# Optimization experiments

Measured on AMD Instinct MI355X. Metric: run time of the kernel, lower is better.

Reference implementation:

```python
import jax, jax.numpy as jnp
import numpy as np

B, C, H, G, NCLS = 32, 256, 128, 128, 2  # graphs, nodes-per-graph==in_channels, hidden, matrix pool, classes
N = B * C                                # total nodes = 8192
E = 131072


def setup_inputs() -> dict:
    key = jax.random.key(0)
    ks = jax.random.split(key, 12)
    gain = 5.0 / 3.0
    xav = gain * np.sqrt(6.0 / (C + C))  # xavier_uniform bound for [C,C]
    return {
        "x": jax.random.normal(ks[0], (N, C), jnp.float32),
        "edge_index": jax.random.randint(ks[1], (2, E), 0, N),
        "graph_id": jax.random.randint(ks[2], (B,), 0, G),
        "batch": jnp.arange(N) // C,
        "pert_W": jax.random.uniform(ks[3], (G, C, C), jnp.float32, -xav, xav),
        "pert_b": jax.random.uniform(ks[4], (G, C, C), jnp.float32, -xav, xav),
        "mask_W": jax.random.uniform(ks[5], (G, C, C), jnp.float32, -xav, xav),
        "gcn_w0": jax.random.normal(ks[6], (C, H), jnp.float32) / np.sqrt(C),
        "gcn_w1": jax.random.normal(ks[7], (H, H), jnp.float32) / np.sqrt(H),
        "gcn_w2": jax.random.normal(ks[8], (H, H), jnp.float32) / np.sqrt(H),
        "mlp_W": jax.random.normal(ks[9], (2 * H, NCLS), jnp.float32) / np.sqrt(2 * H),
        "mlp_b": jnp.zeros((NCLS,), jnp.float32),
    }


def _hard_where(s):
    # MyWhere: 0 if s <= 0.5 else 1
    return jnp.where(s <= 0.5, 0.0, 1.0).astype(s.dtype)


def _predictor(x, adj, batch, gcn_w0, gcn_w1, gcn_w2, mlp_W, mlp_b):
    # GCN encoder: h <- relu(A @ h @ W); readout = concat(mean-pool, max-pool); MLP+sigmoid
    h = x
    for W in (gcn_w0, gcn_w1, gcn_w2):
        h = jax.nn.relu(adj @ (h @ W))
    sums = jax.ops.segment_sum(h, batch, num_segments=B)
    cnt = jax.ops.segment_sum(jnp.ones((h.shape[0], 1), h.dtype), batch, num_segments=B)
    mean = sums / jnp.maximum(cnt, 1.0)
    mx = jax.ops.segment_max(h, batch, num_segments=B)
    pooled = jnp.concatenate([mean, mx], axis=-1)  # [B, 2H]
    return jax.nn.sigmoid(pooled @ mlp_W + mlp_b)


def reference(x, edge_index, graph_id, batch, pert_W, pert_b, mask_W,
              gcn_w0, gcn_w1, gcn_w2, mlp_W, mlp_b):
    # dense adjacency (duplicate edges sum, matching sparse_coo.to_dense)
    adj = jnp.zeros((N, N), jnp.float32).at[edge_index[0], edge_index[1]].add(1.0)
    P = pert_W[graph_id]    # [B, C, C] block-diag blocks
    bias = pert_b[graph_id]  # [B, C, C] block-diag bias blocks
    # block_diag(P) @ adj == per-block GEMM over row stripes
    PA = jnp.einsum('bij,bjn->bin', P, adj.reshape(B, C, N))  # [B, C, N]
    PA = PA.reshape(B, C, B, C).at[jnp.arange(B), :, jnp.arange(B), :].add(bias)
    PA = PA.reshape(N, N)
    pert_adj = _hard_where(jax.nn.sigmoid(PA))
    M = _hard_where(jax.nn.sigmoid(mask_W[graph_id].reshape(N, C)))
    x_masked = M * x
    pred = _predictor(x, adj, batch, gcn_w0, gcn_w1, gcn_w2, mlp_W, mlp_b)
    aug_pred = _predictor(x_masked, pert_adj, batch, gcn_w0, gcn_w1, gcn_w2, mlp_W, mlp_b)
    return (adj, pert_adj, M, pred, aug_pred, x_masked)
```

## Files before the change

kernel.cpp:

```cpp
#include <hip/hip_runtime.h>
#include <hip/hip_bf16.h>

#define NN 8192
#define CC 256
#define BBg 32
#define HH 128
#define EE 131072

typedef __attribute__((ext_vector_type(8))) short short8;
typedef __attribute__((ext_vector_type(4))) float f32x4;
typedef unsigned long long ull;

__device__ __forceinline__ float hard01(float v) {
    if (v >= 1e-6f) return 1.0f;
    if (v <= 0.0f) return 0.0f;
    float ef = (float)exp(-(double)v);
    float s = 1.0f / (1.0f + ef);
    return (s > 0.5f) ? 1.0f : 0.0f;
}

__device__ __forceinline__ unsigned short f2bf(float f) {
    unsigned u = __float_as_uint(f);
    u += 0x7FFFu + ((u >> 16) & 1u);
    return (unsigned short)(u >> 16);
}
__device__ __forceinline__ float bf2f(unsigned short b) {
    return __uint_as_float(((unsigned)b) << 16);
}

__global__ void k_hist(const int* __restrict__ ei, int* __restrict__ rowcnt,
                       int* __restrict__ colcnt, unsigned char* __restrict__ coljs) {
    int e = blockIdx.x * 256 + threadIdx.x;
    if (e >= EE) return;
    int r = ei[e], c = ei[EE + e];
    atomicAdd(&rowcnt[r], 1);
    int idx = (r >> 8) * NN + c;
    int slot = atomicAdd(&colcnt[idx], 1);
    if (slot < 16) coljs[(size_t)idx * 16 + slot] = (unsigned char)(r & 255);
}

__global__ void k_scan(const int* __restrict__ rowcnt, int* __restrict__ rowptr,
                       int* __restrict__ rowfill) {
    __shared__ int sums[256];
    int t = threadIdx.x;
    int base = t * 32;
    int loc[32];
    int s = 0;
    #pragma unroll
    for (int i = 0; i < 32; ++i) { loc[i] = s; s += rowcnt[base + i]; }
    sums[t] = s;
    __syncthreads();
    if (t == 0) {
        int a = 0;
        for (int i = 0; i < 256; ++i) { int v = sums[i]; sums[i] = a; a += v; }
        rowptr[NN] = a;
    }
    __syncthreads();
    int off = sums[t];
    #pragma unroll
    for (int i = 0; i < 32; ++i) {
        rowptr[base + i] = off + loc[i];
        rowfill[base + i] = off + loc[i];
    }
}

__global__ void k_fill(const int* __restrict__ ei, int* __restrict__ rowfill,
                       int* __restrict__ csrcol) {
    int e = blockIdx.x * 256 + threadIdx.x;
    if (e >= EE) return;
    int r = ei[e], c = ei[EE + e];
    int pos = atomicAdd(&rowfill[r], 1);
    csrcol[pos] = c;
}

__global__ void __launch_bounds__(256) k_adj_write(const int* __restrict__ rowptr,
                                                   const int* __restrict__ csrcol,
                                                   float* __restrict__ adj) {
    __shared__ int cnt[NN];
    int row = blockIdx.x, t = threadIdx.x;
    int4 z = make_int4(0, 0, 0, 0);
    #pragma unroll
    for (int i = 0; i < 8; ++i) *(int4*)&cnt[(i * 256 + t) * 4] = z;
    __syncthreads();
    int start = rowptr[row], end = rowptr[row + 1];
    for (int e = start + t; e < end; e += 256) atomicAdd(&cnt[csrcol[e]], 1);
    __syncthreads();
    float* dst = adj + (size_t)row * NN;
    #pragma unroll
    for (int i = 0; i < 8; ++i) {
        int p = i * 1024 + t * 4;
        float4 f;
        f.x = (float)cnt[p + 0]; f.y = (float)cnt[p + 1];
        f.z = (float)cnt[p + 2]; f.w = (float)cnt[p + 3];
        *(float4*)(dst + p) = f;
    }
}

__global__ void k_mask(const float* __restrict__ maskW, const int* __restrict__ gid,
                       const float* __restrict__ x, float* __restrict__ Mo,
                       float* __restrict__ xm) {
    int i = blockIdx.x * 256 + threadIdx.x;
    int base = i * 4;
    int r = base >> 8;
    int c = base & 255;
    int g = gid[r >> 8];
    float4 mv = *(const float4*)(maskW + ((size_t)g << 16) + ((size_t)(r & 255) << 8) + c);
    float4 xv = *(const float4*)(x + ((size_t)r << 8) + c);
    float4 m, o;
    m.x = hard01(mv.x); m.y = hard01(mv.y); m.z = hard01(mv.z); m.w = hard01(mv.w);
    o.x = m.x * xv.x; o.y = m.y * xv.y; o.z = m.z * xv.z; o.w = m.w * xv.w;
    *(float4*)(Mo + ((size_t)r << 8) + c) = m;
    *(float4*)(xm + ((size_t)r << 8) + c) = o;
}

__global__ void __launch_bounds__(256) k_pertadj(const float* __restrict__ pertW,
                                                 const float* __restrict__ pertB,
                                                 const int* __restrict__ gid,
                                                 const int* __restrict__ colcnt,
                                                 const unsigned char* __restrict__ coljs,
                                                 float* __restrict__ padj,
                                                 unsigned char* __restrict__ padjbits) {
    __shared__ float Pl[32][257];
    int nc = blockIdx.x & 3, rt = (blockIdx.x >> 2) & 7, b = blockIdx.x >> 5;
    int t = threadIdx.x;
    int g = gid[b];
    const float* src = pertW + ((size_t)g << 16) + (size_t)rt * 32 * CC;
    #pragma unroll 4
    for (int i = 0; i < 32; ++i) Pl[i][t] = src[i * CC + t];
    __syncthreads();
    int ty = t >> 6, tx = t & 63;
    int ro = ty * 8;
    const float* bsrc = pertB + ((size_t)g << 16) + (size_t)(rt * 32 + ro) * CC;
    for (int it = 0; it < 4; ++it) {
        unsigned bits[8];
        #pragma unroll
        for (int ii = 0; ii < 8; ++ii) bits[ii] = 0;
        #pragma unroll
        for (int half = 0; half < 2; ++half) {
            int n = nc * 2048 + it * 512 + tx * 8 + half * 4;
            int cidx = b * NN + n;
            int4 cnt4 = *(const int4*)(colcnt + cidx);
            const uint4* jp = (const uint4*)(coljs + (size_t)cidx * 16);
            float s[8][4];
            #pragma unroll
            for (int ii = 0; ii < 8; ++ii)
                #pragma unroll
                for (int cc = 0; cc < 4; ++cc) s[ii][cc] = 0.0f;
            #pragma unroll
            for (int cc = 0; cc < 4; ++cc) {
                int cnt = (&cnt4.x)[cc];
                cnt = cnt > 16 ? 16 : cnt;
                if (cnt == 0) continue;
                uint4 jv = jp[cc];
                for (int q = 0; q < cnt; ++q) {
                    unsigned word = (q < 8) ? ((q < 4) ? jv.x : jv.y)
                                            : ((q < 12) ? jv.z : jv.w);
                    int j = (word >> ((q & 3) * 8)) & 255;
                    #pragma unroll
                    for (int ii = 0; ii < 8; ++ii) s[ii][cc] += Pl[ro + ii][j];
                }
            }
            bool diag = ((n >> 8) == b);
            #pragma unroll
            for (int ii = 0; ii < 8; ++ii) {
                float4 v = make_float4(s[ii][0], s[ii][1], s[ii][2], s[ii][3]);
                if (diag) {
                    float4 bv = *(const float4*)(bsrc + (size_t)ii * CC + (n & 255));
                    v.x += bv.x; v.y += bv.y; v.z += bv.z; v.w += bv.w;
                }
                float4 f;
                f.x = hard01(v.x); f.y = hard01(v.y); f.z = hard01(v.z); f.w = hard01(v.w);
                size_t ob = (size_t)(b * CC + rt * 32 + ro + ii) * NN + n;
                *(float4*)(padj + ob) = f;
                unsigned nib = (f.x != 0.f ? 1u : 0u) | (f.y != 0.f ? 2u : 0u) |
                               (f.z != 0.f ? 4u : 0u) | (f.w != 0.f ? 8u : 0u);
                bits[ii] |= nib << (half * 4);
            }
        }
        #pragma unroll
        for (int ii = 0; ii < 8; ++ii) {
            size_t bb = (size_t)(b * CC + rt * 32 + ro + ii) * (NN / 8)
                        + nc * 256 + it * 64 + tx;
            padjbits[bb] = (unsigned char)bits[ii];
        }
    }
}

__global__ void __launch_bounds__(256) k_gemm_dual(const float* __restrict__ Ap,
                                                   const float* __restrict__ Aa,
                                                   const float* __restrict__ W,
                                                   float* __restrict__ Zp,
                                                   unsigned short* __restrict__ Zthi,
                                                   unsigned short* __restrict__ Ztlo,
                                                   int K, int relu, int aparts, int apstride) {
    __shared__ float Alp[32][68];
    __shared__ float Ala[32][68];
    __shared__ float Wl[64][132];
    int mt = blockIdx.x;
    int t = threadIdx.x;
    int ty = t >> 3, tx = t & 7;
    float accp[16], acca[16];
    #pragma unroll
    for (int u = 0; u < 16; ++u) { accp[u] = 0.0f; acca[u] = 0.0f; }
    for (int kc = 0; kc < K; kc += 64) {
        int row = t >> 3, q = t & 7;
        {
            const float* ap = Ap + (size_t)(mt * 32 + row) * K + kc + q * 8;
            float4 f0 = *(const float4*)ap;
            float4 f1 = *(const float4*)(ap + 4);
            if (relu) {
                f0.x = fmaxf(f0.x, 0.f); f0.y = fmaxf(f0.y, 0.f);
                f0.z = fmaxf(f0.z, 0.f); f0.w = fmaxf(f0.w, 0.f);
                f1.x = fmaxf(f1.x, 0.f); f1.y = fmaxf(f1.y, 0.f);
                f1.z = fmaxf(f1.z, 0.f); f1.w = fmaxf(f1.w, 0.f);
            }
            *(float4*)&Alp[row][q * 8] = f0;
            *(float4*)&Alp[row][q * 8 + 4] = f1;
        }
        {
            const float* ap = Aa + (size_t)(mt * 32 + row) * K + kc + q * 8;
            float4 f0 = *(const float4*)ap;
            float4 f1 = *(const float4*)(ap + 4);
            for (int p = 1; p < aparts; ++p) {
                float4 g0 = *(const float4*)(ap + (size_t)p * apstride);
                float4 g1 = *(const float4*)(ap + (size_t)p * apstride + 4);
                f0.x += g0.x; f0.y += g0.y; f0.z += g0.z; f0.w += g0.w;
                f1.x += g1.x; f1.y += g1.y; f1.z += g1.z; f1.w += g1.w;
            }
            if (relu) {
                f0.x = fmaxf(f0.x, 0.f); f0.y = fmaxf(f0.y, 0.f);
                f0.z = fmaxf(f0.z, 0.f); f0.w = fmaxf(f0.w, 0.f);
                f1.x = fmaxf(f1.x, 0.f); f1.y = fmaxf(f1.y, 0.f);
                f1.z = fmaxf(f1.z, 0.f); f1.w = fmaxf(f1.w, 0.f);
            }
            *(float4*)&Ala[row][q * 8] = f0;
            *(float4*)&Ala[row][q * 8 + 4] = f1;
        }
        {
            int wrow = t >> 2, wq = t & 3;
            const float* wp = W + (size_t)(kc + wrow) * HH + wq * 32;
            #pragma unroll
            for (int u = 0; u < 32; u += 4)
                *(float4*)&Wl[wrow][wq * 32 + u] = *(const float4*)(wp + u);
        }
        __syncthreads();
        #pragma unroll 2
        for (int kk = 0; kk < 64; ++kk) {
            float a = Alp[ty][kk];
            float b2 = Ala[ty][kk];
            #pragma unroll
            for (int u = 0; u < 16; u += 4) {
                float4 wv = *(const float4*)(&Wl[kk][tx * 16 + u]);
                accp[u + 0] += a * wv.x; accp[u + 1] += a * wv.y;
                accp[u + 2] += a * wv.z; accp[u + 3] += a * wv.w;
                acca[u + 0] += b2 * wv.x; acca[u + 1] += b2 * wv.y;
                acca[u + 2] += b2 * wv.z; acca[u + 3] += b2 * wv.w;
            }
        }
        __syncthreads();
    }
    {
        float* cp = Zp + (size_t)(mt * 32 + ty) * HH + tx * 16;
        #pragma unroll
        for (int u = 0; u < 16; u += 4) {
            float4 f;
            f.x = accp[u]; f.y = accp[u + 1]; f.z = accp[u + 2]; f.w = accp[u + 3];
            *(float4*)(cp + u) = f;
        }
    }
    {
        __syncthreads();
        float* Tl = &Wl[0][0];
        #pragma unroll
        for (int u = 0; u < 16; ++u) Tl[ty * 132 + tx * 16 + u] = acca[u];
        __syncthreads();
        int col = t >> 1, half = t & 1;
        unsigned short hu[16] __attribute__((aligned(16)));
        unsigned short lu[16] __attribute__((aligned(16)));
        #pragma unroll
        for (int rr = 0; rr < 16; ++rr) {
            float v = Tl[(half * 16 + rr) * 132 + col];
            unsigned short hb = f2bf(v);
            hu[rr] = hb;
            lu[rr] = f2bf(v - bf2f(hb));
        }
        size_t ob = (size_t)col * NN + mt * 32 + half * 16;
        *(uint4*)(Zthi + ob)     = *(const uint4*)&hu[0];
        *(uint4*)(Zthi + ob + 8) = *(const uint4*)&hu[8];
        *(uint4*)(Ztlo + ob)     = *(const uint4*)&lu[0];
        *(uint4*)(Ztlo + ob + 8) = *(const uint4*)&lu[8];
    }
}

__global__ void k_spmm_gather(const int* __restrict__ rowptr,
                              const int* __restrict__ csrcol,
                              const float* __restrict__ Z,
                              float* __restrict__ S) {
    int t = threadIdx.x;
    int row = blockIdx.x * 2 + (t >> 7);
    int col = t & 127;
    int start = rowptr[row], end = rowptr[row + 1];
    float s = 0.f;
    if (start < end) {
        int c = csrcol[start];
        for (int e = start; e < end; ++e) {
            int cn = (e + 1 < end) ? csrcol[e + 1] : 0;
            s += Z[(size_t)c * HH + col];
            c = cn;
        }
    }
    S[(size_t)row * HH + col] = s;
}

__global__ void __launch_bounds__(256) k_mfma_spmm(const unsigned char* __restrict__ padjbits,
                                                   const unsigned short* __restrict__ Zthi,
                                                   const unsigned short* __restrict__ Ztlo,
                                                   float* __restrict__ Sp) {
    __shared__ unsigned short Bh[128 * 72];
    __shared__ unsigned short Bl[128 * 72];
    int mt = blockIdx.x >> 3, sk = blockIdx.x & 7;
    int t = threadIdx.x, w = t >> 6, lane = t & 63;
    int quad = lane >> 4, l15 = lane & 15;
    f32x4 acc[2][8];
    #pragma unroll
    for (int m = 0; m < 2; ++m)
        #pragma unroll
        for (int i = 0; i < 8; ++i) acc[m][i] = (f32x4){0.f, 0.f, 0.f, 0.f};
    int bn = t >> 1, bq = t & 1;
    const unsigned short* zh = Zthi + (size_t)bn * NN + bq * 32;
    const unsigned short* zl = Ztlo + (size_t)bn * NN + bq * 32;
    int row0 = mt * 128 + w * 32 + l15;
    const ull* ab0 = (const ull*)(padjbits + (size_t)row0 * (NN / 8) + sk * 128);
    const ull* ab1 = (const ull*)(padjbits + (size_t)(row0 + 16) * (NN / 8) + sk * 128);
    int ldsw = bn * 72 + bq * 32;
    int bmb = l15 * 72 + quad * 8;
    for (int st = 0; st < 16; ++st) {
        int k = sk * 1024 + st * 64;
        ull bits0 = ab0[st];
        ull bits1 = ab1[st];
        *(uint4*)(Bh + ldsw + 0)  = *(const uint4*)(zh + k);
        *(uint4*)(Bh + ldsw + 8)  = *(const uint4*)(zh + k + 8);
        *(uint4*)(Bh + ldsw + 16) = *(const uint4*)(zh + k + 16);
        *(uint4*)(Bh + ldsw + 24) = *(const uint4*)(zh + k + 24);
        *(uint4*)(Bl + ldsw + 0)  = *(const uint4*)(zl + k);
        *(uint4*)(Bl + ldsw + 8)  = *(const uint4*)(zl + k + 8);
        *(uint4*)(Bl + ldsw + 16) = *(const uint4*)(zl + k + 16);
        *(uint4*)(Bl + ldsw + 24) = *(const uint4*)(zl + k + 24);
        __syncthreads();
        #pragma unroll
        for (int ksub = 0; ksub < 2; ++ksub) {
            unsigned b0 = ((unsigned)(bits0 >> (ksub * 32)) >> (quad * 8)) & 0xFFu;
            unsigned b1 = ((unsigned)(bits1 >> (ksub * 32)) >> (quad * 8)) & 0xFFu;
            short8 a0, a1;
            #pragma unroll
            for (int j = 0; j < 8; ++j) {
                a0[j] = (b0 & (1u << j)) ? (short)0x3F80 : (short)0;
                a1[j] = (b1 & (1u << j)) ? (short)0x3F80 : (short)0;
            }
            #pragma unroll
            for (int nt = 0; nt < 8; ++nt) {
                short8 fh = *(const short8*)(Bh + nt * 16 * 72 + bmb + ksub * 32);
                short8 fl = *(const short8*)(Bl + nt * 16 * 72 + bmb + ksub * 32);
                acc[0][nt] = __builtin_amdgcn_mfma_f32_16x16x32_bf16(a0, fh, acc[0][nt], 0, 0, 0);
                acc[0][nt] = __builtin_amdgcn_mfma_f32_16x16x32_bf16(a0, fl, acc[0][nt], 0, 0, 0);
                acc[1][nt] = __builtin_amdgcn_mfma_f32_16x16x32_bf16(a1, fh, acc[1][nt], 0, 0, 0);
                acc[1][nt] = __builtin_amdgcn_mfma_f32_16x16x32_bf16(a1, fl, acc[1][nt], 0, 0, 0);
            }
        }
        __syncthreads();
    }
    int dc = l15, dr = quad * 4;
    float* base = Sp + (size_t)sk * NN * HH + (size_t)(mt * 128 + w * 32 + dr) * HH;
    #pragma unroll
    for (int m = 0; m < 2; ++m)
        #pragma unroll
        for (int nt = 0; nt < 8; ++nt)
            #pragma unroll
            for (int r = 0; r < 4; ++r)
                base[(size_t)(m * 16 + r) * HH + nt * 16 + dc] = acc[m][nt][r];
}

__global__ void __launch_bounds__(256) k_pool2(const float* __restrict__ S,
                                               const float* __restrict__ Sp,
                                               const float* __restrict__ mlpW,
                                               const float* __restrict__ mlpb,
                                               float* __restrict__ pred,
                                               float* __restrict__ augp,
                                               int apstride) {
    __shared__ float ps[256], pm[256], pl[256], r0[256], r1[256];
    int aug = blockIdx.x >> 5, g = blockIdx.x & 31, t = threadIdx.x;
    const float* Sb = aug ? Sp : S;
    int parts = aug ? 8 : 1;
    float* outp = aug ? augp : pred;
    int col = t & 127, half = t >> 7;
    const float* base = Sb + (size_t)(g * CC + half * 128) * HH + col;
    float sum = 0.f, mx = -3.0e38f;
    for (int rr = 0; rr < 128; ++rr) {
        float v = base[(size_t)rr * HH];
        for (int p = 1; p < parts; ++p) v += base[(size_t)p * apstride + (size_t)rr * HH];
        v = fmaxf(v, 0.f);
        sum += v;
        mx = fmaxf(mx, v);
    }
    ps[t] = sum; pm[t] = mx;
    __syncthreads();
    if (half == 0) {
        pl[col] = (ps[col] + ps[col + 128]) * (1.0f / 256.0f);
        pl[col + 128] = fmaxf(pm[col], pm[col + 128]);
    }
    __syncthreads();
    r0[t] = pl[t] * mlpW[t * 2 + 0];
    r1[t] = pl[t] * mlpW[t * 2 + 1];
    __syncthreads();
    for (int sft = 128; sft > 0; sft >>= 1) {
        if (t < sft) { r0[t] += r0[t + sft]; r1[t] += r1[t + sft]; }
        __syncthreads();
    }
    if (t == 0) {
        float l0 = r0[0] + mlpb[0];
        float l1 = r1[0] + mlpb[1];
        outp[g * 2 + 0] = 1.0f / (1.0f + expf(-l0));
        outp[g * 2 + 1] = 1.0f / (1.0f + expf(-l1));
    }
}

extern "C" void kernel_launch(void* const* d_in, const int* in_sizes, int n_in,
                              void* d_out, int out_size, void* d_ws, size_t ws_size,
                              hipStream_t stream) {
    (void)in_sizes; (void)n_in; (void)out_size; (void)ws_size;
    const float* x     = (const float*)d_in[0];
    const int*   ei    = (const int*)d_in[1];
    const int*   gid   = (const int*)d_in[2];
    const float* pertW = (const float*)d_in[4];
    const float* pertB = (const float*)d_in[5];
    const float* maskW = (const float*)d_in[6];
    const float* w0    = (const float*)d_in[7];
    const float* w1    = (const float*)d_in[8];
    const float* w2    = (const float*)d_in[9];
    const float* mlpW  = (const float*)d_in[10];
    const float* mlpb  = (const float*)d_in[11];

    float* out  = (float*)d_out;
    float* adj  = out;
    float* padj = out + (size_t)NN * NN;
    float* Mo   = out + 2 * (size_t)NN * NN;
    float* pred = Mo + (size_t)NN * CC;
    float* augp = pred + (size_t)BBg * 2;
    float* xm   = augp + (size_t)BBg * 2;

    char* ws = (char*)d_ws;
    int*            colcnt   = (int*)ws;
    int*            rowcnt   = (int*)(ws + (1 << 20));
    int*            rowptr   = (int*)(ws + (1 << 20) + (64 << 10));
    int*            rowfill  = (int*)(ws + (1 << 20) + (128 << 10));
    unsigned char*  coljs    = (unsigned char*)(ws + (2 << 20));
    int*            csrcol   = (int*)(ws + (6 << 20));
    float*          Z        = (float*)(ws + (7 << 20));
    float*          S        = (float*)(ws + (11 << 20));
    unsigned short* Zthi     = (unsigned short*)(ws + (15 << 20));
    unsigned short* Ztlo     = (unsigned short*)(ws + (17 << 20));
    float*          Sp       = (float*)(ws + (19 << 20));
    unsigned char*  padjbits = (unsigned char*)(ws + (51 << 20));
    const int PS = NN * HH;

    hipMemsetAsync(colcnt, 0, (1 << 20) + (32 << 10), stream);
    k_hist<<<EE / 256, 256, 0, stream>>>(ei, rowcnt, colcnt, coljs);
    k_scan<<<1, 256, 0, stream>>>(rowcnt, rowptr, rowfill);
    k_fill<<<EE / 256, 256, 0, stream>>>(ei, rowfill, csrcol);
    k_adj_write<<<NN, 256, 0, stream>>>(rowptr, csrcol, adj);
    k_mask<<<(NN * CC / 4) / 256, 256, 0, stream>>>(maskW, gid, x, Mo, xm);
    k_pertadj<<<1024, 256, 0, stream>>>(pertW, pertB, gid, colcnt, coljs, padj, padjbits);

    k_gemm_dual<<<256, 256, 0, stream>>>(x, xm, w0, Z, Zthi, Ztlo, 256, 0, 1, 0);
    k_spmm_gather<<<NN / 2, 256, 0, stream>>>(rowptr, csrcol, Z, S);
    k_mfma_spmm<<<512, 256, 0, stream>>>(padjbits, Zthi, Ztlo, Sp);
    k_gemm_dual<<<256, 256, 0, stream>>>(S, Sp, w1, Z, Zthi, Ztlo, 128, 1, 8, PS);
    k_spmm_gather<<<NN / 2, 256, 0, stream>>>(rowptr, csrcol, Z, S);
    k_mfma_spmm<<<512, 256, 0, stream>>>(padjbits, Zthi, Ztlo, Sp);
    k_gemm_dual<<<256, 256, 0, stream>>>(S, Sp, w2, Z, Zthi, Ztlo, 128, 1, 8, PS);
    k_spmm_gather<<<NN / 2, 256, 0, stream>>>(rowptr, csrcol, Z, S);
    k_mfma_spmm<<<512, 256, 0, stream>>>(padjbits, Zthi, Ztlo, Sp);
    k_pool2<<<64, 256, 0, stream>>>(S, Sp, mlpW, mlpb, pred, augp, PS);
}
```

Baseline: 1.104 ms.

## Double-buffer MFMA SpMM with larger row tiles; restructure pertadj epilogue and gather unroll

The bit-matrix MFMA SpMM now handles 256 rows per block (4 M-subtiles per wave) with a 32-wide K step and double-buffered LDS. The next Z tile and adjacency bits are prefetched into registers while the current tile is multiplied, which removes one barrier per step and reuses each B fragment across more rows. The perturbed-adjacency kernel now accumulates all 8 columns before running a single epilogue that writes one bit byte and two float4 stores. The CSR gather loop is unrolled by two with independent accumulators. The cost is higher register pressure from 32 accumulator tiles and only 256 blocks in the SpMM launch, which may lower occupancy.

```diff
diff --git a/kernel.cpp b/kernel.cpp
--- a/kernel.cpp
+++ b/kernel.cpp
@@ -132,20 +132,18 @@
     int ro = ty * 8;
     const float* bsrc = pertB + ((size_t)g << 16) + (size_t)(rt * 32 + ro) * CC;
     for (int it = 0; it < 4; ++it) {
-        unsigned bits[8];
-        #pragma unroll
-        for (int ii = 0; ii < 8; ++ii) bits[ii] = 0;
+        int n0 = nc * 2048 + it * 512 + tx * 8;
+        float s[8][8];
+        #pragma unroll
+        for (int ii = 0; ii < 8; ++ii)
+            #pragma unroll
+            for (int cc = 0; cc < 8; ++cc) s[ii][cc] = 0.0f;
         #pragma unroll
         for (int half = 0; half < 2; ++half) {
-            int n = nc * 2048 + it * 512 + tx * 8 + half * 4;
+            int n = n0 + half * 4;
             int cidx = b * NN + n;
             int4 cnt4 = *(const int4*)(colcnt + cidx);
             const uint4* jp = (const uint4*)(coljs + (size_t)cidx * 16);
-            float s[8][4];
-            #pragma unroll
-            for (int ii = 0; ii < 8; ++ii)
-                #pragma unroll
-                for (int cc = 0; cc < 4; ++cc) s[ii][cc] = 0.0f;
             #pragma unroll
             for (int cc = 0; cc < 4; ++cc) {
                 int cnt = (&cnt4.x)[cc];
@@ -157,31 +155,34 @@
                                             : ((q < 12) ? jv.z : jv.w);
                     int j = (word >> ((q & 3) * 8)) & 255;
                     #pragma unroll
-                    for (int ii = 0; ii < 8; ++ii) s[ii][cc] += Pl[ro + ii][j];
+                    for (int ii = 0; ii < 8; ++ii) s[ii][half * 4 + cc] += Pl[ro + ii][j];
                 }
             }
-            bool diag = ((n >> 8) == b);
-            #pragma unroll
-            for (int ii = 0; ii < 8; ++ii) {
-                float4 v = make_float4(s[ii][0], s[ii][1], s[ii][2], s[ii][3]);
-                if (diag) {
-                    float4 bv = *(const float4*)(bsrc + (size_t)ii * CC + (n & 255));
-                    v.x += bv.x; v.y += bv.y; v.z += bv.z; v.w += bv.w;
-                }
-                float4 f;
-                f.x = hard01(v.x); f.y = hard01(v.y); f.z = hard01(v.z); f.w = hard01(v.w);
-                size_t ob = (size_t)(b * CC + rt * 32 + ro + ii) * NN + n;
-                *(float4*)(padj + ob) = f;
-                unsigned nib = (f.x != 0.f ? 1u : 0u) | (f.y != 0.f ? 2u : 0u) |
-                               (f.z != 0.f ? 4u : 0u) | (f.w != 0.f ? 8u : 0u);
-                bits[ii] |= nib << (half * 4);
-            }
-        }
+        }
+        bool diag = ((n0 >> 8) == b);
         #pragma unroll
         for (int ii = 0; ii < 8; ++ii) {
+            if (diag) {
+                const float* bp = bsrc + (size_t)ii * CC + (n0 & 255);
+                #pragma unroll
+                for (int cc = 0; cc < 8; ++cc) s[ii][cc] += bp[cc];
+            }
+            float f[8];
+            unsigned byte = 0;
+            #pragma unroll
+            for (int cc = 0; cc < 8; ++cc) {
+                f[cc] = hard01(s[ii][cc]);
+                if (f[cc] != 0.f) byte |= (1u << cc);
+            }
+            size_t ob = (size_t)(b * CC + rt * 32 + ro + ii) * NN + n0;
+            float4 f0, f1;
+            f0.x = f[0]; f0.y = f[1]; f0.z = f[2]; f0.w = f[3];
+            f1.x = f[4]; f1.y = f[5]; f1.z = f[6]; f1.w = f[7];
+            *(float4*)(padj + ob) = f0;
+            *(float4*)(padj + ob + 4) = f1;
             size_t bb = (size_t)(b * CC + rt * 32 + ro + ii) * (NN / 8)
                         + nc * 256 + it * 64 + tx;
-            padjbits[bb] = (unsigned char)bits[ii];
+            padjbits[bb] = (unsigned char)byte;
         }
     }
 }
@@ -300,79 +301,97 @@
     int row = blockIdx.x * 2 + (t >> 7);
     int col = t & 127;
     int start = rowptr[row], end = rowptr[row + 1];
-    float s = 0.f;
-    if (start < end) {
-        int c = csrcol[start];
-        for (int e = start; e < end; ++e) {
-            int cn = (e + 1 < end) ? csrcol[e + 1] : 0;
-            s += Z[(size_t)c * HH + col];
-            c = cn;
-        }
-    }
-    S[(size_t)row * HH + col] = s;
+    float s0 = 0.f, s1 = 0.f;
+    int e = start;
+    for (; e + 2 <= end; e += 2) {
+        int c0 = csrcol[e], c1 = csrcol[e + 1];
+        s0 += Z[(size_t)c0 * HH + col];
+        s1 += Z[(size_t)c1 * HH + col];
+    }
+    if (e < end) s0 += Z[(size_t)csrcol[e] * HH + col];
+    S[(size_t)row * HH + col] = s0 + s1;
 }
 
 __global__ void __launch_bounds__(256) k_mfma_spmm(const unsigned char* __restrict__ padjbits,
                                                    const unsigned short* __restrict__ Zthi,
                                                    const unsigned short* __restrict__ Ztlo,
                                                    float* __restrict__ Sp) {
-    __shared__ unsigned short Bh[128 * 72];
-    __shared__ unsigned short Bl[128 * 72];
+    __shared__ unsigned short Bh[2][128 * 40];
+    __shared__ unsigned short Bl[2][128 * 40];
     int mt = blockIdx.x >> 3, sk = blockIdx.x & 7;
     int t = threadIdx.x, w = t >> 6, lane = t & 63;
     int quad = lane >> 4, l15 = lane & 15;
-    f32x4 acc[2][8];
-    #pragma unroll
-    for (int m = 0; m < 2; ++m)
+    f32x4 acc[4][8];
+    #pragma unroll
+    for (int m = 0; m < 4; ++m)
         #pragma unroll
         for (int i = 0; i < 8; ++i) acc[m][i] = (f32x4){0.f, 0.f, 0.f, 0.f};
     int bn = t >> 1, bq = t & 1;
-    const unsigned short* zh = Zthi + (size_t)bn * NN + bq * 32;
-    const unsigned short* zl = Ztlo + (size_t)bn * NN + bq * 32;
-    int row0 = mt * 128 + w * 32 + l15;
-    const ull* ab0 = (const ull*)(padjbits + (size_t)row0 * (NN / 8) + sk * 128);
-    const ull* ab1 = (const ull*)(padjbits + (size_t)(row0 + 16) * (NN / 8) + sk * 128);
-    int ldsw = bn * 72 + bq * 32;
-    int bmb = l15 * 72 + quad * 8;
-    for (int st = 0; st < 16; ++st) {
-        int k = sk * 1024 + st * 64;
-        ull bits0 = ab0[st];
-        ull bits1 = ab1[st];
-        *(uint4*)(Bh + ldsw + 0)  = *(const uint4*)(zh + k);
-        *(uint4*)(Bh + ldsw + 8)  = *(const uint4*)(zh + k + 8);
-        *(uint4*)(Bh + ldsw + 16) = *(const uint4*)(zh + k + 16);
-        *(uint4*)(Bh + ldsw + 24) = *(const uint4*)(zh + k + 24);
-        *(uint4*)(Bl + ldsw + 0)  = *(const uint4*)(zl + k);
-        *(uint4*)(Bl + ldsw + 8)  = *(const uint4*)(zl + k + 8);
-        *(uint4*)(Bl + ldsw + 16) = *(const uint4*)(zl + k + 16);
-        *(uint4*)(Bl + ldsw + 24) = *(const uint4*)(zl + k + 24);
+    const unsigned short* zh = Zthi + (size_t)bn * NN + sk * 1024 + bq * 16;
+    const unsigned short* zl = Ztlo + (size_t)bn * NN + sk * 1024 + bq * 16;
+    int row0 = mt * 256 + w * 64 + l15;
+    const unsigned* ab[4];
+    #pragma unroll
+    for (int m = 0; m < 4; ++m)
+        ab[m] = (const unsigned*)(padjbits + (size_t)(row0 + m * 16) * (NN / 8)) + sk * 32;
+    int ldsw = bn * 40 + bq * 16;
+    int bmb = l15 * 40 + quad * 8;
+    uint4 rh0, rh1, rl0, rl1;
+    unsigned bits[4], nbits[4];
+    rh0 = *(const uint4*)(zh + 0);
+    rh1 = *(const uint4*)(zh + 8);
+    rl0 = *(const uint4*)(zl + 0);
+    rl1 = *(const uint4*)(zl + 8);
+    #pragma unroll
+    for (int m = 0; m < 4; ++m) bits[m] = ab[m][0];
+    *(uint4*)(&Bh[0][ldsw + 0]) = rh0;
+    *(uint4*)(&Bh[0][ldsw + 8]) = rh1;
+    *(uint4*)(&Bl[0][ldsw + 0]) = rl0;
+    *(uint4*)(&Bl[0][ldsw + 8]) = rl1;
+    __syncthreads();
+    for (int st = 0; st < 32; ++st) {
+        int cur = st & 1;
+        if (st < 31) {
+            int k = (st + 1) * 32;
+            rh0 = *(const uint4*)(zh + k);
+            rh1 = *(const uint4*)(zh + k + 8);
+            rl0 = *(const uint4*)(zl + k);
+            rl1 = *(const uint4*)(zl + k + 8);
+            #pragma unroll
+            for (int m = 0; m < 4; ++m) nbits[m] = ab[m][st + 1];
+        }
+        short8 a[4];
+        #pragma unroll
+        for (int m = 0; m < 4; ++m) {
+            unsigned byte = (bits[m] >> (quad * 8)) & 0xFFu;
+            #pragma unroll
+            for (int j = 0; j < 8; ++j)
+                a[m][j] = (byte & (1u << j)) ? (short)0x3F80 : (short)0;
+        }
+        #pragma unroll
+        for (int nt = 0; nt < 8; ++nt) {
+            short8 fh = *(const short8*)(&Bh[cur][nt * 16 * 40 + bmb]);
+            short8 fl = *(const short8*)(&Bl[cur][nt * 16 * 40 + bmb]);
+            #pragma unroll
+            for (int m = 0; m < 4; ++m) {
+                acc[m][nt] = __builtin_amdgcn_mfma_f32_16x16x32_bf16(a[m], fh, acc[m][nt], 0, 0, 0);
+                acc[m][nt] = __builtin_amdgcn_mfma_f32_16x16x32_bf16(a[m], fl, acc[m][nt], 0, 0, 0);
+            }
+        }
+        if (st < 31) {
+            *(uint4*)(&Bh[1 - cur][ldsw + 0]) = rh0;
+            *(uint4*)(&Bh[1 - cur][ldsw + 8]) = rh1;
+            *(uint4*)(&Bl[1 - cur][ldsw + 0]) = rl0;
+            *(uint4*)(&Bl[1 - cur][ldsw + 8]) = rl1;
+            #pragma unroll
+            for (int m = 0; m < 4; ++m) bits[m] = nbits[m];
+        }
         __syncthreads();
-        #pragma unroll
-        for (int ksub = 0; ksub < 2; ++ksub) {
-            unsigned b0 = ((unsigned)(bits0 >> (ksub * 32)) >> (quad * 8)) & 0xFFu;
-            unsigned b1 = ((unsigned)(bits1 >> (ksub * 32)) >> (quad * 8)) & 0xFFu;
-            short8 a0, a1;
-            #pragma unroll
-            for (int j = 0; j < 8; ++j) {
-                a0[j] = (b0 & (1u << j)) ? (short)0x3F80 : (short)0;
-                a1[j] = (b1 & (1u << j)) ? (short)0x3F80 : (short)0;
-            }
-            #pragma unroll
-            for (int nt = 0; nt < 8; ++nt) {
-                short8 fh = *(const short8*)(Bh + nt * 16 * 72 + bmb + ksub * 32);
-                short8 fl = *(const short8*)(Bl + nt * 16 * 72 + bmb + ksub * 32);
-                acc[0][nt] = __builtin_amdgcn_mfma_f32_16x16x32_bf16(a0, fh, acc[0][nt], 0, 0, 0);
-                acc[0][nt] = __builtin_amdgcn_mfma_f32_16x16x32_bf16(a0, fl, acc[0][nt], 0, 0, 0);
-                acc[1][nt] = __builtin_amdgcn_mfma_f32_16x16x32_bf16(a1, fh, acc[1][nt], 0, 0, 0);
-                acc[1][nt] = __builtin_amdgcn_mfma_f32_16x16x32_bf16(a1, fl, acc[1][nt], 0, 0, 0);
-            }
-        }
-        __syncthreads();
     }
     int dc = l15, dr = quad * 4;
-    float* base = Sp + (size_t)sk * NN * HH + (size_t)(mt * 128 + w * 32 + dr) * HH;
-    #pragma unroll
-    for (int m = 0; m < 2; ++m)
+    float* base = Sp + (size_t)sk * NN * HH + (size_t)(mt * 256 + w * 64 + dr) * HH;
+    #pragma unroll
+    for (int m = 0; m < 4; ++m)
         #pragma unroll
         for (int nt = 0; nt < 8; ++nt)
             #pragma unroll
@@ -473,12 +492,12 @@
 
     k_gemm_dual<<<256, 256, 0, stream>>>(x, xm, w0, Z, Zthi, Ztlo, 256, 0, 1, 0);
     k_spmm_gather<<<NN / 2, 256, 0, stream>>>(rowptr, csrcol, Z, S);
-    k_mfma_spmm<<<512, 256, 0, stream>>>(padjbits, Zthi, Ztlo, Sp);
+    k_mfma_spmm<<<256, 256, 0, stream>>>(padjbits, Zthi, Ztlo, Sp);
     k_gemm_dual<<<256, 256, 0, stream>>>(S, Sp, w1, Z, Zthi, Ztlo, 128, 1, 8, PS);
     k_spmm_gather<<<NN / 2, 256, 0, stream>>>(rowptr, csrcol, Z, S);
-    k_mfma_spmm<<<512, 256, 0, stream>>>(padjbits, Zthi, Ztlo, Sp);
+    k_mfma_spmm<<<256, 256, 0, stream>>>(padjbits, Zthi, Ztlo, Sp);
     k_gemm_dual<<<256, 256, 0, stream>>>(S, Sp, w2, Z, Zthi, Ztlo, 128, 1, 8, PS);
     k_spmm_gather<<<NN / 2, 256, 0, stream>>>(rowptr, csrcol, Z, S);
-    k_mfma_spmm<<<512, 256, 0, stream>>>(padjbits, Zthi, Ztlo, Sp);
+    k_mfma_spmm<<<256, 256, 0, stream>>>(padjbits, Zthi, Ztlo, Sp);
     k_pool2<<<64, 256, 0, stream>>>(S, Sp, mlpW, mlpb, pred, augp, PS);
 }
```

New measurement: 1.064 ms. 1.04x faster.
